# Optimization experiments

Measured on AMD Instinct MI355X. Metric: run time of the kernel, lower is better.

Reference implementation:

```python
import jax, jax.numpy as jnp
import numpy as np

N = 50000      # n_points (== n_support, non-strided)
H = 32         # neighbors per point
IN_F = 128
OUT_F = 256
MID = OUT_F // 4   # bottleneck width = 64
K = 15         # kernel points
RADIUS = 2.0
KP_EXTENT = 1.2 * RADIUS / 5.0  # config.KP_extent * radius / density_parameter
EPS = 1e-6
SLOPE = 0.1


def _wvar(k, size):
    # weight_variable: normal(scale=sqrt(2/size[-1])), zeroed outside 2*std
    std = np.sqrt(2.0 / size[-1])
    w = jax.random.normal(k, size, jnp.float32) * std
    return jnp.where(jnp.abs(w) > 2.0 * std, 0.0, w)


def setup_inputs():
    key = jax.random.key(0)
    ks = jax.random.split(key, 12)
    query_points = jax.random.uniform(ks[0], (N, 3), jnp.float32)
    support_points = query_points  # non-strided: same cloud
    neighbors_indices = jax.random.randint(ks[1], (N, H), 0, N, jnp.int32)
    features = jax.random.normal(ks[2], (N, IN_F), jnp.float32)
    kp = (jax.random.uniform(ks[3], (K, 3), jnp.float32) * 2.0 - 1.0) * (0.66 * KP_EXTENT)
    kernel_points = kp.at[0].set(0.0)  # fixed_kernel_points='center'
    w1 = _wvar(ks[4], (IN_F, MID))
    kw = _wvar(ks[5], (K, MID, MID))
    w3 = _wvar(ks[6], (MID, OUT_F))
    ws = _wvar(ks[7], (IN_F, OUT_F))
    def bnp(k, c):
        k1, k2 = jax.random.split(k)
        g = jax.random.uniform(k1, (c,), jnp.float32, 0.75, 1.25)
        b = jax.random.normal(k2, (c,), jnp.float32) * 0.1
        return g, b
    g1, b1 = bnp(ks[8], MID)
    g2, b2 = bnp(ks[9], MID)
    g3, b3 = bnp(ks[10], OUT_F)
    gs, bs = bnp(ks[11], OUT_F)
    return dict(query_points=query_points, support_points=support_points,
                neighbors_indices=neighbors_indices, features=features,
                kernel_points=kernel_points, w1=w1, g1=g1, b1=b1,
                kw=kw, g2=g2, b2=b2, w3=w3, g3=g3, b3=b3, ws=ws, gs=gs, bs=bs)


def _bn(x, g, b):
    # BatchNorm1d in training mode: batch statistics over points, biased var
    m = jnp.mean(x, 0)
    v = jnp.var(x, 0)
    return g * (x - m) * jax.lax.rsqrt(v + EPS) + b


def _lrelu(x):
    return jnp.where(x >= 0, x, SLOPE * x)


def _unary(x, w, g, b):
    return _lrelu(_bn(x @ w, g, b))


def _kpconv(q, s, inds, f, kp, kw):
    # pad support with a far shadow point and features with a zero row (faithful to KPConv)
    s_pad = jnp.concatenate([s, jnp.full((1, 3), 1e6, s.dtype)], 0)
    f_pad = jnp.concatenate([f, jnp.zeros((1, f.shape[1]), f.dtype)], 0)
    neigh = s_pad[inds]                        # [n,h,3] gather
    d = neigh - q[:, None, :]                  # [n,h,3]
    sq = jnp.sum((d[:, :, None, :] - kp[None, None, :, :]) ** 2, -1)  # [n,h,K]
    dist = jnp.sqrt(jnp.maximum(sq, 1e-12))
    infl = jnp.maximum(0.0, 1.0 - dist / KP_EXTENT)   # 'linear' KP_influence
    nf = f_pad[inds]                           # [n,h,d] gather
    wf = jnp.einsum('nhk,nhd->nkd', infl, nf)  # aggregate over neighbors
    return jnp.einsum('nkd,kdo->no', wf, kw)   # 'sum' aggregation over kernel pts


def reference(query_points, support_points, neighbors_indices, features, kernel_points,
              w1, g1, b1, kw, g2, b2, w3, g3, b3, ws, gs, bs):
    x = _unary(features, w1, g1, b1)                                     # conv1
    x = _lrelu(_bn(_kpconv(query_points, support_points, neighbors_indices,
                           x, kernel_points, kw), g2, b2))               # conv2 (KPConv)
    x = _unary(x, w3, g3, b3)                                            # conv3
    sc = _unary(features, ws, gs, bs)                                    # shortcut (non-strided)
    return _lrelu(sc + x)
```

## Files before the change

kernel.cpp:

```cpp
#include <hip/hip_runtime.h>

#define NPTS 50000
#define HN 32
#define INF1 128
#define OUTF3 256
#define MIDF 64
#define KP 15
#define EPSV 1e-6f
#define SLOPE 0.1f
#define KPE 0.48f
#define INVN (1.f / 50000.f)

typedef __attribute__((ext_vector_type(8))) short short8;
typedef __attribute__((ext_vector_type(4))) float float4v;
typedef unsigned short ushort;
typedef unsigned long long ull;

__device__ inline ushort f2bf(float f) {
    union { float f; unsigned u; } v; v.f = f;
    unsigned r = v.u + 0x7fff + ((v.u >> 16) & 1);
    return (ushort)(r >> 16);
}
__device__ inline float bf2f(ushort u) {
    union { unsigned u; float f; } v; v.u = ((unsigned)u) << 16;
    return v.f;
}


__global__ __launch_bounds__(256)
void k_repack_all(const float* __restrict__ w1, const float* __restrict__ wsw,
                  ushort* __restrict__ wpC,
                  const float* __restrict__ kw, ushort* __restrict__ wpk,
                  const float* __restrict__ w3, ushort* __restrict__ wp3) {
    int id = blockIdx.x * 256 + threadIdx.x;
    if (id < 5120) {
        int l = id & 63;
        int nt = (id >> 6) % 20, s = id / 1280;
        int n = nt * 16 + (l & 15);
        int k0 = s * 32 + ((l >> 4) & 3) * 8;
#pragma unroll
        for (int j = 0; j < 8; j++) {
            float v = (n < 64) ? w1[(k0 + j) * 64 + n] : wsw[(k0 + j) * 256 + (n - 64)];
            wpC[id * 8 + j] = f2bf(v);
        }
    } else if (id < 13312) {
        int id2 = id - 5120;
        int l2 = id2 & 63;
        int nt = (id2 >> 6) & 3, s = id2 >> 8;
        int n = nt * 16 + (l2 & 15);
        int kd0 = s * 32 + ((l2 >> 4) & 3) * 8;
#pragma unroll
        for (int j = 0; j < 8; j++) {
            int kd = kd0 + j, d = kd >> 4, kk = kd & 15;
            float v = (kk < KP) ? kw[kk * 4096 + d * 64 + n] : 0.f;
            wpk[id2 * 8 + j] = f2bf(v);
        }
    } else if (id < 15360) {
        int id3 = id - 13312;
        int l3 = id3 & 63;
        int nt = (id3 >> 6) % 16, s = id3 / 1024;
        int n = nt * 16 + (l3 & 15);
        int k0 = s * 32 + ((l3 >> 4) & 3) * 8;
#pragma unroll
        for (int j = 0; j < 8; j++)
            wp3[id3 * 8 + j] = f2bf(w3[(k0 + j) * 256 + n]);
    }
}

__global__ __launch_bounds__(256)
void k_conv1sc(const float* __restrict__ feat, const ushort* __restrict__ WpC,
               ushort* __restrict__ x1raw, ushort* __restrict__ scb,
               float* __restrict__ Sa1, float* __restrict__ Sq1,
               float* __restrict__ SaS, float* __restrict__ SqS, int M) {
    __shared__ float sred[320], qred[320];
    int t = threadIdx.x;
    int w = t >> 6, l = t & 63;
    int dl = l & 15, q4 = l >> 4;

    for (int c = t; c < 320; c += 256) { sred[c] = 0.f; qred[c] = 0.f; }
    __syncthreads();

    int m0 = blockIdx.x * 64 + w * 16;
    int row = m0 + dl;
    long arow = (row < M) ? row : (M - 1);
    const float* ap0 = feat + arow * INF1 + q4 * 8;
    short8 afr[4];
#pragma unroll
    for (int s = 0; s < 4; s++) {
        float4 a0 = *(const float4*)(ap0 + s * 32);
        float4 a1 = *(const float4*)(ap0 + s * 32 + 4);
        union { short8 v; ushort u[8]; } au;
        au.u[0] = f2bf(a0.x); au.u[1] = f2bf(a0.y); au.u[2] = f2bf(a0.z); au.u[3] = f2bf(a0.w);
        au.u[4] = f2bf(a1.x); au.u[5] = f2bf(a1.y); au.u[6] = f2bf(a1.z); au.u[7] = f2bf(a1.w);
        afr[s] = au.v;
    }
    const short8* Bp = (const short8*)WpC + l;
    int rb = q4 * 4;
    float sv8[4], sv9[4];
#pragma unroll
    for (int half = 0; half < 2; half++) {
        float4v acc[10];
#pragma unroll
        for (int j = 0; j < 10; j++) acc[j] = (float4v){0.f, 0.f, 0.f, 0.f};
#pragma unroll
        for (int s = 0; s < 4; s++)
#pragma unroll
            for (int j = 0; j < 10; j++) {
                short8 bf = Bp[(s * 20 + half * 10 + j) * 64];
                acc[j] = __builtin_amdgcn_mfma_f32_16x16x32_bf16(afr[s], bf, acc[j], 0, 0, 0);
            }
#pragma unroll
        for (int r = 0; r < 4; r++) {
            int rr = m0 + rb + r;
            if (rr < M) {
                if (half == 0) {
                    ull pk = 0;
#pragma unroll
                    for (int j = 0; j < 4; j++)
                        pk |= ((ull)f2bf(acc[j][r])) << (16 * j);
                    *(ull*)(x1raw + (long)rr * 64 + 4 * dl) = pk;
                    ull p0 = 0;
#pragma unroll
                    for (int e = 0; e < 4; e++)
                        p0 |= ((ull)f2bf(acc[4 + e][r])) << (16 * e);
                    *(ull*)(scb + (long)rr * 256 + dl * 4) = p0;
                } else {
                    ull p1 = (ull)f2bf(sv8[r]) | ((ull)f2bf(sv9[r]) << 16)
                           | ((ull)f2bf(acc[0][r]) << 32) | ((ull)f2bf(acc[1][r]) << 48);
                    *(ull*)(scb + (long)rr * 256 + 64 + dl * 4) = p1;
                    ull p2 = 0, p3 = 0;
#pragma unroll
                    for (int e = 0; e < 4; e++) {
                        p2 |= ((ull)f2bf(acc[2 + e][r])) << (16 * e);
                        p3 |= ((ull)f2bf(acc[6 + e][r])) << (16 * e);
                    }
                    *(ull*)(scb + (long)rr * 256 + 128 + dl * 4) = p2;
                    *(ull*)(scb + (long)rr * 256 + 192 + dl * 4) = p3;
                }
            }
        }
        if (half == 0) {
#pragma unroll
            for (int r = 0; r < 4; r++) { sv8[r] = acc[8][r]; sv9[r] = acc[9][r]; }
        }
#pragma unroll
        for (int j = 0; j < 10; j++) {
            float s = 0.f, q = 0.f;
#pragma unroll
            for (int r = 0; r < 4; r++) {
                float v = ((m0 + rb + r) < M) ? acc[j][r] : 0.f;
                s += v; q += v * v;
            }
            s += __shfl_xor(s, 16); s += __shfl_xor(s, 32);
            q += __shfl_xor(q, 16); q += __shfl_xor(q, 32);
            if (q4 == 0) {
                atomicAdd(&sred[(half * 10 + j) * 16 + dl], s);
                atomicAdd(&qred[(half * 10 + j) * 16 + dl], q);
            }
        }
    }
    __syncthreads();
    for (int c = t; c < 320; c += 256) {
        if (c < 64) { atomicAdd(&Sa1[c], sred[c]); atomicAdd(&Sq1[c], qred[c]); }
        else        { atomicAdd(&SaS[c - 64], sred[c]); atomicAdd(&SqS[c - 64], qred[c]); }
    }
}

__global__ __launch_bounds__(256)
void k_bnx(const ushort* __restrict__ X, ushort* __restrict__ Y,
           const float* __restrict__ Sa, const float* __restrict__ Sq,
           const float* __restrict__ g, const float* __restrict__ b) {
    __shared__ float sc[64], sh[64];
    int t = threadIdx.x;
    if (t < 64) {
        float m = Sa[t] * INVN;
        float v = Sq[t] * INVN - m * m;
        float s = g[t] * rsqrtf(v + EPSV);
        sc[t] = s; sh[t] = b[t] - s * m;
    }
    __syncthreads();
    int i = blockIdx.x * 256 + t;
    long base = (long)i * 4;
    int dlp = i & 15;
    ull vin = *(const ull*)(X + base);
    ull vout = 0;
#pragma unroll
    for (int j = 0; j < 4; j++) {
        int c = j * 16 + dlp;
        float f = bf2f((ushort)((vin >> (16 * j)) & 0xffff));
        float v = f * sc[c] + sh[c];
        v = (v >= 0.f) ? v : SLOPE * v;
        vout |= ((ull)f2bf(v)) << (16 * j);
    }
    *(ull*)(Y + base) = vout;
}

__global__ __launch_bounds__(256)
void k_kpconv(const float* __restrict__ qpts, const float* __restrict__ spts,
              const int* __restrict__ nbr, const ushort* __restrict__ x1b,
              const float* __restrict__ kpp, const ushort* __restrict__ kwp,
              ushort* __restrict__ y, float* __restrict__ Sa, float* __restrict__ Sq) {
    __shared__ __align__(16) ushort wfs[16][1032];
    __shared__ float posd[4][4][3][HN];

    int t = threadIdx.x;
    int w = t >> 6, l = t & 63;
    int dl = l & 15, q4 = l >> 4;

    int kmin = (dl < KP) ? dl : (KP - 1);
    float kx = kpp[kmin * 3 + 0], ky = kpp[kmin * 3 + 1], kz = kpp[kmin * 3 + 2];

    int nb = blockIdx.x * 16 + w * 4;

    if (l < HN) {
        int mi[4];
#pragma unroll
        for (int pp = 0; pp < 4; pp++)
            mi[pp] = nbr[(long)(nb + pp) * HN + l];
#pragma unroll
        for (int pp = 0; pp < 4; pp++) {
            float px = spts[(long)mi[pp] * 3 + 0];
            float py = spts[(long)mi[pp] * 3 + 1];
            float pz = spts[(long)mi[pp] * 3 + 2];
            posd[w][pp][0][l] = px - qpts[(nb + pp) * 3 + 0];
            posd[w][pp][1][l] = py - qpts[(nb + pp) * 3 + 1];
            posd[w][pp][2][l] = pz - qpts[(nb + pp) * 3 + 2];
        }
    }

    uint2 rj[2][8];
    {
        const int4* np = (const int4*)(nbr + (long)nb * HN + q4 * 8);
        int4 ia = np[0], ib = np[1];
        int id[8] = {ia.x, ia.y, ia.z, ia.w, ib.x, ib.y, ib.z, ib.w};
#pragma unroll
        for (int j = 0; j < 8; j++)
            rj[0][j] = *(const uint2*)(x1b + (long)id[j] * MIDF + 4 * dl);
    }

#pragma unroll
    for (int pp = 0; pp < 4; pp++) {
        if (pp < 3) {
            const int4* np = (const int4*)(nbr + (long)(nb + pp + 1) * HN + q4 * 8);
            int4 ia = np[0], ib = np[1];
            int id[8] = {ia.x, ia.y, ia.z, ia.w, ib.x, ib.y, ib.z, ib.w};
#pragma unroll
            for (int j = 0; j < 8; j++)
                rj[(pp + 1) & 1][j] = *(const uint2*)(x1b + (long)id[j] * MIDF + 4 * dl);
        }

        union { float4 v; float f[4]; } px0, px1, py0, py1, pz0, pz1;
        px0.v = *(const float4*)&posd[w][pp][0][q4 * 8];
        px1.v = *(const float4*)&posd[w][pp][0][q4 * 8 + 4];
        py0.v = *(const float4*)&posd[w][pp][1][q4 * 8];
        py1.v = *(const float4*)&posd[w][pp][1][q4 * 8 + 4];
        pz0.v = *(const float4*)&posd[w][pp][2][q4 * 8];
        pz1.v = *(const float4*)&posd[w][pp][2][q4 * 8 + 4];

        union { short8 v; ushort u8[8]; } afr;
#pragma unroll
        for (int j = 0; j < 8; j++) {
            float ex = ((j < 4) ? px0.f[j & 3] : px1.f[j & 3]) - kx;
            float ey = ((j < 4) ? py0.f[j & 3] : py1.f[j & 3]) - ky;
            float ez = ((j < 4) ? pz0.f[j & 3] : pz1.f[j & 3]) - kz;
            float sq = ex * ex + ey * ey + ez * ez;
            float dist = sqrtf(fmaxf(sq, 1e-12f));
            float inf = fmaxf(0.f, 1.f - dist * (1.f / KPE));
            afr.u8[j] = (dl < KP) ? f2bf(inf) : (ushort)0;
        }

        union { short8 v; unsigned d[4]; } bfr[4];
#pragma unroll
        for (int dj = 0; dj < 4; dj++) {
            unsigned a_lo = rj[pp & 1][2 * dj].x, b_lo = rj[pp & 1][2 * dj + 1].x;
            unsigned a_hi = rj[pp & 1][2 * dj].y, b_hi = rj[pp & 1][2 * dj + 1].y;
            bfr[0].d[dj] = __builtin_amdgcn_perm(b_lo, a_lo, 0x05040100u);
            bfr[1].d[dj] = __builtin_amdgcn_perm(b_lo, a_lo, 0x07060302u);
            bfr[2].d[dj] = __builtin_amdgcn_perm(b_hi, a_hi, 0x05040100u);
            bfr[3].d[dj] = __builtin_amdgcn_perm(b_hi, a_hi, 0x07060302u);
        }

        float4v wfa[4];
#pragma unroll
        for (int nt = 0; nt < 4; nt++)
            wfa[nt] = __builtin_amdgcn_mfma_f32_16x16x32_bf16(
                afr.v, bfr[nt].v, (float4v){0.f, 0.f, 0.f, 0.f}, 0, 0, 0);

        int p = w * 4 + pp;
#pragma unroll
        for (int nt = 0; nt < 4; nt++) {
            ull pk = 0;
#pragma unroll
            for (int r = 0; r < 4; r++) {
                ushort hv = ((q4 * 4 + r) < KP) ? f2bf(wfa[nt][r]) : (ushort)0;
                pk |= ((ull)hv) << (16 * r);
            }
            *(ull*)(&wfs[p][(nt * 16 + dl) * 16 + q4 * 4]) = pk;
        }
    }
    __syncthreads();

    float4v acc0 = (float4v){0.f, 0.f, 0.f, 0.f};
    float4v acc1 = (float4v){0.f, 0.f, 0.f, 0.f};
    const ushort* arow = &wfs[dl][0] + q4 * 8;
    const short8* Bp = (const short8*)kwp + l;
#pragma unroll
    for (int s = 0; s < 32; s += 2) {
        short8 a0 = *(const short8*)(arow + s * 32);
        short8 b0 = Bp[(s * 4 + w) * 64];
        acc0 = __builtin_amdgcn_mfma_f32_16x16x32_bf16(a0, b0, acc0, 0, 0, 0);
        short8 a1 = *(const short8*)(arow + (s + 1) * 32);
        short8 b1 = Bp[((s + 1) * 4 + w) * 64];
        acc1 = __builtin_amdgcn_mfma_f32_16x16x32_bf16(a1, b1, acc1, 0, 0, 0);
    }
    float4v acc = acc0 + acc1;

    int o = w * 16 + dl;
    float s = 0.f, q = 0.f;
#pragma unroll
    for (int r = 0; r < 4; r++) {
        float v = acc[r];
        y[(long)(blockIdx.x * 16 + q4 * 4 + r) * MIDF + o] = f2bf(v);
        s += v; q += v * v;
    }
    s += __shfl_xor(s, 16); s += __shfl_xor(s, 32);
    q += __shfl_xor(q, 16); q += __shfl_xor(q, 32);
    if (q4 == 0) {
        atomicAdd(&Sa[o], s);
        atomicAdd(&Sq[o], q);
    }
}

__global__ __launch_bounds__(256)
void k_conv3(const ushort* __restrict__ x2raw, const ushort* __restrict__ Wp,
             ushort* __restrict__ x3b,
             const float* __restrict__ Sa2, const float* __restrict__ Sq2,
             const float* __restrict__ g2, const float* __restrict__ b2,
             float* __restrict__ Sa3, float* __restrict__ Sq3, int M) {
    __shared__ float sred[256], qred[256];
    __shared__ float scs[64], shs[64];
    int t = threadIdx.x;
    int w = t >> 6, l = t & 63;
    int dl = l & 15, q4 = l >> 4;

    if (t < 64) {
        float m = Sa2[t] * INVN;
        float v = Sq2[t] * INVN - m * m;
        float s = g2[t] * rsqrtf(v + EPSV);
        scs[t] = s; shs[t] = b2[t] - s * m;
    }
    sred[t] = 0.f; qred[t] = 0.f;
    __syncthreads();

    int m0 = blockIdx.x * 64 + w * 16;
    int row = m0 + dl;
    long arow = (row < M) ? row : (M - 1);
    const ushort* ap0 = x2raw + arow * MIDF + q4 * 8;
    short8 au2[2];
#pragma unroll
    for (int s = 0; s < 2; s++) {
        union { short8 v; ushort u[8]; } raw, cv;
        raw.v = *(const short8*)(ap0 + s * 32);
#pragma unroll
        for (int e = 0; e < 8; e++) {
            int d = s * 32 + q4 * 8 + e;
            float f = bf2f(raw.u[e]) * scs[d] + shs[d];
            f = (f >= 0.f) ? f : SLOPE * f;
            cv.u[e] = f2bf(f);
        }
        au2[s] = cv.v;
    }
    const short8* Bp = (const short8*)Wp + l;
    int rb = q4 * 4;
#pragma unroll
    for (int half = 0; half < 2; half++) {
        float4v acc[8];
#pragma unroll
        for (int j = 0; j < 8; j++) acc[j] = (float4v){0.f, 0.f, 0.f, 0.f};
#pragma unroll
        for (int s = 0; s < 2; s++)
#pragma unroll
            for (int j = 0; j < 8; j++) {
                short8 bf = Bp[(s * 16 + half * 8 + j) * 64];
                acc[j] = __builtin_amdgcn_mfma_f32_16x16x32_bf16(au2[s], bf, acc[j], 0, 0, 0);
            }
#pragma unroll
        for (int r = 0; r < 4; r++) {
            int rr = m0 + rb + r;
            if (rr < M) {
#pragma unroll
                for (int g = 0; g < 2; g++) {
                    ull pk = 0;
#pragma unroll
                    for (int e = 0; e < 4; e++)
                        pk |= ((ull)f2bf(acc[g * 4 + e][r])) << (16 * e);
                    *(ull*)(x3b + (long)rr * 256 + (half * 2 + g) * 64 + dl * 4) = pk;
                }
            }
        }
#pragma unroll
        for (int j = 0; j < 8; j++) {
            float s = 0.f, q = 0.f;
#pragma unroll
            for (int r = 0; r < 4; r++) {
                float v = ((m0 + rb + r) < M) ? acc[j][r] : 0.f;
                s += v; q += v * v;
            }
            s += __shfl_xor(s, 16); s += __shfl_xor(s, 32);
            q += __shfl_xor(q, 16); q += __shfl_xor(q, 32);
            if (q4 == 0) {
                atomicAdd(&sred[(half * 8 + j) * 16 + dl], s);
                atomicAdd(&qred[(half * 8 + j) * 16 + dl], q);
            }
        }
    }
    __syncthreads();
    atomicAdd(&Sa3[t], sred[t]);
    atomicAdd(&Sq3[t], qred[t]);
}

__global__ __launch_bounds__(256)
void k_final(const ushort* __restrict__ x3b, const ushort* __restrict__ scb,
             float* __restrict__ out,
             const float* __restrict__ a3, const float* __restrict__ q3,
             const float* __restrict__ g3, const float* __restrict__ b3,
             const float* __restrict__ aS, const float* __restrict__ qS,
             const float* __restrict__ gs, const float* __restrict__ bs) {
    __shared__ float s3[256], h3[256], sS[256], hS[256];
    int t = threadIdx.x;
    {
        float m = a3[t] * INVN;
        float v = q3[t] * INVN - m * m;
        float s = g3[t] * rsqrtf(v + EPSV);
        s3[t] = s; h3[t] = b3[t] - s * m;
        m = aS[t] * INVN;
        v = qS[t] * INVN - m * m;
        s = gs[t] * rsqrtf(v + EPSV);
        sS[t] = s; hS[t] = bs[t] - s * m;
    }
    __syncthreads();
    int ci = blockIdx.x * 256 + t;
    long i = (long)ci * 4;
    int li = ci & 63;
    int cbase = ((li >> 4) << 6) + (li & 15);
    long rowb = (long)(ci >> 6) * 256;
    ull va = *(const ull*)(x3b + i);
    ull vb = *(const ull*)(scb + i);
#pragma unroll
    for (int j = 0; j < 4; j++) {
        int c = cbase + j * 16;
        float x = bf2f((ushort)((va >> (16 * j)) & 0xffff)) * s3[c] + h3[c];
        x = (x >= 0.f) ? x : SLOPE * x;
        float sc = bf2f((ushort)((vb >> (16 * j)) & 0xffff)) * sS[c] + hS[c];
        sc = (sc >= 0.f) ? sc : SLOPE * sc;
        float v = x + sc;
        out[rowb + c] = (v >= 0.f) ? v : SLOPE * v;
    }
}

extern "C" void kernel_launch(void* const* d_in, const int* in_sizes, int n_in,
                              void* d_out, int out_size, void* d_ws, size_t ws_size,
                              hipStream_t stream) {
    const float* qp   = (const float*)d_in[0];
    const float* sp   = (const float*)d_in[1];
    const int*   nbr  = (const int*)d_in[2];
    const float* feat = (const float*)d_in[3];
    const float* kpp  = (const float*)d_in[4];
    const float* w1   = (const float*)d_in[5];
    const float* g1   = (const float*)d_in[6];
    const float* b1   = (const float*)d_in[7];
    const float* kw   = (const float*)d_in[8];
    const float* g2   = (const float*)d_in[9];
    const float* b2   = (const float*)d_in[10];
    const float* w3   = (const float*)d_in[11];
    const float* g3   = (const float*)d_in[12];
    const float* b3   = (const float*)d_in[13];
    const float* wsw  = (const float*)d_in[14];
    const float* gs   = (const float*)d_in[15];
    const float* bs   = (const float*)d_in[16];
    float* out = (float*)d_out;

    char* base = (char*)d_ws;
    ushort* x1raw = (ushort*)(base + 0);
    ushort* x1b   = (ushort*)(base + 6400000);
    ushort* x2raw = (ushort*)(base + 12800000);
    ushort* x3b   = (ushort*)(base + 19200000);
    ushort* scb   = (ushort*)(base + 44800000);
    ushort* wpC   = (ushort*)(base + 70400000);
    ushort* wpk   = (ushort*)(base + 70481920);
    ushort* wp3   = (ushort*)(base + 70612992);
    float*  st    = (float*)(base + 70645760);
    float* acc1 = st,       *q1 = st + 64;
    float* acc2 = st + 128, *q2 = st + 192;
    float* acc3 = st + 256, *q3 = st + 512;
    float* accS = st + 768, *qS = st + 1024;

    hipMemsetAsync(st, 0, 1280 * sizeof(float), stream);

    k_repack_all<<<60, 256, 0, stream>>>(w1, wsw, wpC, kw, wpk, w3, wp3);

    k_conv1sc<<<782, 256, 0, stream>>>(feat, wpC, x1raw, scb, acc1, q1, accS, qS, NPTS);
    k_bnx<<<3125, 256, 0, stream>>>(x1raw, x1b, acc1, q1, g1, b1);

    k_kpconv<<<NPTS / 16, 256, 0, stream>>>(qp, sp, nbr, x1b, kpp, wpk, x2raw, acc2, q2);

    k_conv3<<<782, 256, 0, stream>>>(x2raw, wp3, x3b, acc2, q2, g2, b2, acc3, q3, NPTS);

    k_final<<<12500, 256, 0, stream>>>(x3b, scb, out, acc3, q3, g3, b3, accS, qS, gs, bs);
}
```

Baseline: 300.8 us.

## Use packed bf16 converts, prefetch kpconv gathers and weights, coalesce final stores

Replaces the scalar software float-to-bf16 rounding with the v_cvt_pk_bf16_f32 instruction in all kernels. In the KPConv kernel it issues all four points' neighbour-feature gathers up front instead of double-buffering them, and splits the position gather across all 64 lanes. It also register-prefetches the kernel-weight B fragments ahead of the MFMA loop. The final kernel stages results through LDS so each thread writes a contiguous float4 rather than scattered 16-float-strided scalars. The cost is higher register pressure in kpconv and dropped zero-masking of padded kernel-point rows, which now relies on zero padding of the repacked weights.

New measurement: 295.8 us. Within noise of the previous version (-1.7%).

```diff
diff --git a/kernel.cpp b/kernel.cpp
--- a/kernel.cpp
+++ b/kernel.cpp
@@ -24,6 +24,11 @@
 __device__ inline float bf2f(ushort u) {
     union { unsigned u; float f; } v; v.u = ((unsigned)u) << 16;
     return v.f;
+}
+__device__ inline unsigned cvt_pk_bf16(float lo, float hi) {
+    unsigned r;
+    asm("v_cvt_pk_bf16_f32 %0, %1, %2" : "=v"(r) : "v"(lo), "v"(hi));
+    return r;
 }
 
 
@@ -89,9 +94,11 @@
     for (int s = 0; s < 4; s++) {
         float4 a0 = *(const float4*)(ap0 + s * 32);
         float4 a1 = *(const float4*)(ap0 + s * 32 + 4);
-        union { short8 v; ushort u[8]; } au;
-        au.u[0] = f2bf(a0.x); au.u[1] = f2bf(a0.y); au.u[2] = f2bf(a0.z); au.u[3] = f2bf(a0.w);
-        au.u[4] = f2bf(a1.x); au.u[5] = f2bf(a1.y); au.u[6] = f2bf(a1.z); au.u[7] = f2bf(a1.w);
+        union { short8 v; unsigned d[4]; } au;
+        au.d[0] = cvt_pk_bf16(a0.x, a0.y);
+        au.d[1] = cvt_pk_bf16(a0.z, a0.w);
+        au.d[2] = cvt_pk_bf16(a1.x, a1.y);
+        au.d[3] = cvt_pk_bf16(a1.z, a1.w);
         afr[s] = au.v;
     }
     const short8* Bp = (const short8*)WpC + l;
@@ -114,28 +121,25 @@
             int rr = m0 + rb + r;
             if (rr < M) {
                 if (half == 0) {
-                    ull pk = 0;
-#pragma unroll
-                    for (int j = 0; j < 4; j++)
-                        pk |= ((ull)f2bf(acc[j][r])) << (16 * j);
-                    *(ull*)(x1raw + (long)rr * 64 + 4 * dl) = pk;
-                    ull p0 = 0;
-#pragma unroll
-                    for (int e = 0; e < 4; e++)
-                        p0 |= ((ull)f2bf(acc[4 + e][r])) << (16 * e);
-                    *(ull*)(scb + (long)rr * 256 + dl * 4) = p0;
+                    uint2 pk;
+                    pk.x = cvt_pk_bf16(acc[0][r], acc[1][r]);
+                    pk.y = cvt_pk_bf16(acc[2][r], acc[3][r]);
+                    *(uint2*)(x1raw + (long)rr * 64 + 4 * dl) = pk;
+                    uint2 p0;
+                    p0.x = cvt_pk_bf16(acc[4][r], acc[5][r]);
+                    p0.y = cvt_pk_bf16(acc[6][r], acc[7][r]);
+                    *(uint2*)(scb + (long)rr * 256 + dl * 4) = p0;
                 } else {
-                    ull p1 = (ull)f2bf(sv8[r]) | ((ull)f2bf(sv9[r]) << 16)
-                           | ((ull)f2bf(acc[0][r]) << 32) | ((ull)f2bf(acc[1][r]) << 48);
-                    *(ull*)(scb + (long)rr * 256 + 64 + dl * 4) = p1;
-                    ull p2 = 0, p3 = 0;
-#pragma unroll
-                    for (int e = 0; e < 4; e++) {
-                        p2 |= ((ull)f2bf(acc[2 + e][r])) << (16 * e);
-                        p3 |= ((ull)f2bf(acc[6 + e][r])) << (16 * e);
-                    }
-                    *(ull*)(scb + (long)rr * 256 + 128 + dl * 4) = p2;
-                    *(ull*)(scb + (long)rr * 256 + 192 + dl * 4) = p3;
+                    uint2 p1, p2, p3;
+                    p1.x = cvt_pk_bf16(sv8[r], sv9[r]);
+                    p1.y = cvt_pk_bf16(acc[0][r], acc[1][r]);
+                    p2.x = cvt_pk_bf16(acc[2][r], acc[3][r]);
+                    p2.y = cvt_pk_bf16(acc[4][r], acc[5][r]);
+                    p3.x = cvt_pk_bf16(acc[6][r], acc[7][r]);
+                    p3.y = cvt_pk_bf16(acc[8][r], acc[9][r]);
+                    *(uint2*)(scb + (long)rr * 256 + 64 + dl * 4) = p1;
+                    *(uint2*)(scb + (long)rr * 256 + 128 + dl * 4) = p2;
+                    *(uint2*)(scb + (long)rr * 256 + 192 + dl * 4) = p3;
                 }
             }
         }
@@ -183,16 +187,18 @@
     long base = (long)i * 4;
     int dlp = i & 15;
     ull vin = *(const ull*)(X + base);
-    ull vout = 0;
+    float vv[4];
 #pragma unroll
     for (int j = 0; j < 4; j++) {
         int c = j * 16 + dlp;
         float f = bf2f((ushort)((vin >> (16 * j)) & 0xffff));
         float v = f * sc[c] + sh[c];
-        v = (v >= 0.f) ? v : SLOPE * v;
-        vout |= ((ull)f2bf(v)) << (16 * j);
-    }
-    *(ull*)(Y + base) = vout;
+        vv[j] = (v >= 0.f) ? v : SLOPE * v;
+    }
+    uint2 vo;
+    vo.x = cvt_pk_bf16(vv[0], vv[1]);
+    vo.y = cvt_pk_bf16(vv[2], vv[3]);
+    *(uint2*)(Y + base) = vo;
 }
 
 __global__ __launch_bounds__(256)
@@ -212,43 +218,44 @@
 
     int nb = blockIdx.x * 16 + w * 4;
 
-    if (l < HN) {
-        int mi[4];
-#pragma unroll
-        for (int pp = 0; pp < 4; pp++)
-            mi[pp] = nbr[(long)(nb + pp) * HN + l];
-#pragma unroll
-        for (int pp = 0; pp < 4; pp++) {
-            float px = spts[(long)mi[pp] * 3 + 0];
-            float py = spts[(long)mi[pp] * 3 + 1];
-            float pz = spts[(long)mi[pp] * 3 + 2];
-            posd[w][pp][0][l] = px - qpts[(nb + pp) * 3 + 0];
-            posd[w][pp][1][l] = py - qpts[(nb + pp) * 3 + 1];
-            posd[w][pp][2][l] = pz - qpts[(nb + pp) * 3 + 2];
-        }
-    }
-
-    uint2 rj[2][8];
+    int idg[4][8];
+#pragma unroll
+    for (int pp = 0; pp < 4; pp++) {
+        const int4* np = (const int4*)(nbr + (long)(nb + pp) * HN + q4 * 8);
+        int4 ia = np[0], ib = np[1];
+        idg[pp][0] = ia.x; idg[pp][1] = ia.y; idg[pp][2] = ia.z; idg[pp][3] = ia.w;
+        idg[pp][4] = ib.x; idg[pp][5] = ib.y; idg[pp][6] = ib.z; idg[pp][7] = ib.w;
+    }
+
     {
-        const int4* np = (const int4*)(nbr + (long)nb * HN + q4 * 8);
-        int4 ia = np[0], ib = np[1];
-        int id[8] = {ia.x, ia.y, ia.z, ia.w, ib.x, ib.y, ib.z, ib.w};
+        int hh = l & 31, hf = l >> 5;
+        float dx[2], dy[2], dz[2];
+#pragma unroll
+        for (int p2 = 0; p2 < 2; p2++) {
+            int pp = hf * 2 + p2;
+            int idx = nbr[(long)(nb + pp) * HN + hh];
+            dx[p2] = spts[(long)idx * 3 + 0] - qpts[(nb + pp) * 3 + 0];
+            dy[p2] = spts[(long)idx * 3 + 1] - qpts[(nb + pp) * 3 + 1];
+            dz[p2] = spts[(long)idx * 3 + 2] - qpts[(nb + pp) * 3 + 2];
+        }
+#pragma unroll
+        for (int p2 = 0; p2 < 2; p2++) {
+            int pp = hf * 2 + p2;
+            posd[w][pp][0][hh] = dx[p2];
+            posd[w][pp][1][hh] = dy[p2];
+            posd[w][pp][2][hh] = dz[p2];
+        }
+    }
+
+    uint2 rj[4][8];
+#pragma unroll
+    for (int pp = 0; pp < 4; pp++)
 #pragma unroll
         for (int j = 0; j < 8; j++)
-            rj[0][j] = *(const uint2*)(x1b + (long)id[j] * MIDF + 4 * dl);
-    }
+            rj[pp][j] = *(const uint2*)(x1b + (long)idg[pp][j] * MIDF + 4 * dl);
 
 #pragma unroll
     for (int pp = 0; pp < 4; pp++) {
-        if (pp < 3) {
-            const int4* np = (const int4*)(nbr + (long)(nb + pp + 1) * HN + q4 * 8);
-            int4 ia = np[0], ib = np[1];
-            int id[8] = {ia.x, ia.y, ia.z, ia.w, ib.x, ib.y, ib.z, ib.w};
-#pragma unroll
-            for (int j = 0; j < 8; j++)
-                rj[(pp + 1) & 1][j] = *(const uint2*)(x1b + (long)id[j] * MIDF + 4 * dl);
-        }
-
         union { float4 v; float f[4]; } px0, px1, py0, py1, pz0, pz1;
         px0.v = *(const float4*)&posd[w][pp][0][q4 * 8];
         px1.v = *(const float4*)&posd[w][pp][0][q4 * 8 + 4];
@@ -257,7 +264,7 @@
         pz0.v = *(const float4*)&posd[w][pp][2][q4 * 8];
         pz1.v = *(const float4*)&posd[w][pp][2][q4 * 8 + 4];
 
-        union { short8 v; ushort u8[8]; } afr;
+        float inf[8];
 #pragma unroll
         for (int j = 0; j < 8; j++) {
             float ex = ((j < 4) ? px0.f[j & 3] : px1.f[j & 3]) - kx;
@@ -265,15 +272,18 @@
             float ez = ((j < 4) ? pz0.f[j & 3] : pz1.f[j & 3]) - kz;
             float sq = ex * ex + ey * ey + ez * ez;
             float dist = sqrtf(fmaxf(sq, 1e-12f));
-            float inf = fmaxf(0.f, 1.f - dist * (1.f / KPE));
-            afr.u8[j] = (dl < KP) ? f2bf(inf) : (ushort)0;
-        }
+            inf[j] = fmaxf(0.f, 1.f - dist * (1.f / KPE));
+        }
+        union { short8 v; unsigned d2[4]; } afr;
+#pragma unroll
+        for (int jj = 0; jj < 4; jj++)
+            afr.d2[jj] = cvt_pk_bf16(inf[2 * jj], inf[2 * jj + 1]);
 
         union { short8 v; unsigned d[4]; } bfr[4];
 #pragma unroll
         for (int dj = 0; dj < 4; dj++) {
-            unsigned a_lo = rj[pp & 1][2 * dj].x, b_lo = rj[pp & 1][2 * dj + 1].x;
-            unsigned a_hi = rj[pp & 1][2 * dj].y, b_hi = rj[pp & 1][2 * dj + 1].y;
+            unsigned a_lo = rj[pp][2 * dj].x, b_lo = rj[pp][2 * dj + 1].x;
+            unsigned a_hi = rj[pp][2 * dj].y, b_hi = rj[pp][2 * dj + 1].y;
             bfr[0].d[dj] = __builtin_amdgcn_perm(b_lo, a_lo, 0x05040100u);
             bfr[1].d[dj] = __builtin_amdgcn_perm(b_lo, a_lo, 0x07060302u);
             bfr[2].d[dj] = __builtin_amdgcn_perm(b_hi, a_hi, 0x05040100u);
@@ -289,29 +299,33 @@
         int p = w * 4 + pp;
 #pragma unroll
         for (int nt = 0; nt < 4; nt++) {
-            ull pk = 0;
-#pragma unroll
-            for (int r = 0; r < 4; r++) {
-                ushort hv = ((q4 * 4 + r) < KP) ? f2bf(wfa[nt][r]) : (ushort)0;
-                pk |= ((ull)hv) << (16 * r);
-            }
-            *(ull*)(&wfs[p][(nt * 16 + dl) * 16 + q4 * 4]) = pk;
-        }
-    }
+            uint2 pk;
+            pk.x = cvt_pk_bf16(wfa[nt][0], wfa[nt][1]);
+            pk.y = cvt_pk_bf16(wfa[nt][2], wfa[nt][3]);
+            *(uint2*)(&wfs[p][(nt * 16 + dl) * 16 + q4 * 4]) = pk;
+        }
+    }
+
+    const short8* Bq = (const short8*)kwp + l;
+    short8 bc0 = Bq[(0 * 4 + w) * 64];
+    short8 bc1 = Bq[(1 * 4 + w) * 64];
     __syncthreads();
 
     float4v acc0 = (float4v){0.f, 0.f, 0.f, 0.f};
     float4v acc1 = (float4v){0.f, 0.f, 0.f, 0.f};
     const ushort* arow = &wfs[dl][0] + q4 * 8;
-    const short8* Bp = (const short8*)kwp + l;
 #pragma unroll
     for (int s = 0; s < 32; s += 2) {
+        short8 bn0, bn1;
+        if (s < 30) {
+            bn0 = Bq[((s + 2) * 4 + w) * 64];
+            bn1 = Bq[((s + 3) * 4 + w) * 64];
+        }
         short8 a0 = *(const short8*)(arow + s * 32);
-        short8 b0 = Bp[(s * 4 + w) * 64];
-        acc0 = __builtin_amdgcn_mfma_f32_16x16x32_bf16(a0, b0, acc0, 0, 0, 0);
         short8 a1 = *(const short8*)(arow + (s + 1) * 32);
-        short8 b1 = Bp[((s + 1) * 4 + w) * 64];
-        acc1 = __builtin_amdgcn_mfma_f32_16x16x32_bf16(a1, b1, acc1, 0, 0, 0);
+        acc0 = __builtin_amdgcn_mfma_f32_16x16x32_bf16(a0, bc0, acc0, 0, 0, 0);
+        acc1 = __builtin_amdgcn_mfma_f32_16x16x32_bf16(a1, bc1, acc1, 0, 0, 0);
+        bc0 = bn0; bc1 = bn1;
     }
     float4v acc = acc0 + acc1;
 
@@ -359,15 +373,19 @@
     short8 au2[2];
 #pragma unroll
     for (int s = 0; s < 2; s++) {
-        union { short8 v; ushort u[8]; } raw, cv;
+        union { short8 v; ushort u[8]; } raw;
+        union { short8 v; unsigned d[4]; } cv;
         raw.v = *(const short8*)(ap0 + s * 32);
+        float fv[8];
 #pragma unroll
         for (int e = 0; e < 8; e++) {
             int d = s * 32 + q4 * 8 + e;
             float f = bf2f(raw.u[e]) * scs[d] + shs[d];
-            f = (f >= 0.f) ? f : SLOPE * f;
-            cv.u[e] = f2bf(f);
-        }
+            fv[e] = (f >= 0.f) ? f : SLOPE * f;
+        }
+#pragma unroll
+        for (int e2 = 0; e2 < 4; e2++)
+            cv.d[e2] = cvt_pk_bf16(fv[2 * e2], fv[2 * e2 + 1]);
         au2[s] = cv.v;
     }
     const short8* Bp = (const short8*)Wp + l;
@@ -390,11 +408,10 @@
             if (rr < M) {
 #pragma unroll
                 for (int g = 0; g < 2; g++) {
-                    ull pk = 0;
-#pragma unroll
-                    for (int e = 0; e < 4; e++)
-                        pk |= ((ull)f2bf(acc[g * 4 + e][r])) << (16 * e);
-                    *(ull*)(x3b + (long)rr * 256 + (half * 2 + g) * 64 + dl * 4) = pk;
+                    uint2 pk;
+                    pk.x = cvt_pk_bf16(acc[g * 4 + 0][r], acc[g * 4 + 1][r]);
+                    pk.y = cvt_pk_bf16(acc[g * 4 + 2][r], acc[g * 4 + 3][r]);
+                    *(uint2*)(x3b + (long)rr * 256 + (half * 2 + g) * 64 + dl * 4) = pk;
                 }
             }
         }
@@ -427,6 +444,7 @@
              const float* __restrict__ aS, const float* __restrict__ qS,
              const float* __restrict__ gs, const float* __restrict__ bs) {
     __shared__ float s3[256], h3[256], sS[256], hS[256];
+    __shared__ __align__(16) float tr[4][256];
     int t = threadIdx.x;
     {
         float m = a3[t] * INVN;
@@ -441,9 +459,9 @@
     __syncthreads();
     int ci = blockIdx.x * 256 + t;
     long i = (long)ci * 4;
-    int li = ci & 63;
+    int li = t & 63;
+    int r = t >> 6;
     int cbase = ((li >> 4) << 6) + (li & 15);
-    long rowb = (long)(ci >> 6) * 256;
     ull va = *(const ull*)(x3b + i);
     ull vb = *(const ull*)(scb + i);
 #pragma unroll
@@ -454,8 +472,11 @@
         float sc = bf2f((ushort)((vb >> (16 * j)) & 0xffff)) * sS[c] + hS[c];
         sc = (sc >= 0.f) ? sc : SLOPE * sc;
         float v = x + sc;
-        out[rowb + c] = (v >= 0.f) ? v : SLOPE * v;
-    }
+        tr[r][c] = (v >= 0.f) ? v : SLOPE * v;
+    }
+    long rowb = (long)(ci >> 6) * 256;
+    float4 o4 = *(const float4*)(&tr[r][li * 4]);
+    *(float4*)(out + rowb + li * 4) = o4;
 }
 
 extern "C" void kernel_launch(void* const* d_in, const int* in_sizes, int n_in,
```
